# Performance work log

Measured on AMD Instinct MI355X. Metric: run time of the kernel, lower is better.

Reference implementation:

```python
import jax, jax.numpy as jnp
import numpy as np

B, F, D, OUT = 1024, 256, 256, 128
EXP = [10, 25]          # expansion_rates
CUM = [1, 10]           # cum_expansion_rates


def setup_inputs() -> dict:
    key = jax.random.key(0)
    ks = jax.random.split(key, 12)
    s = 0.05
    return {
        "h0": jax.random.normal(ks[0], (B, 1, F), jnp.float32),
        "h1": jax.random.normal(ks[1], (B, EXP[0], F), jnp.float32),
        "h2": jax.random.normal(ks[2], (B, EXP[0] * EXP[1], F), jnp.float32),
        "mask0": (jax.random.uniform(ks[3], (B, 1, EXP[0], 1)) < 0.9).astype(jnp.float32),
        "mask1": (jax.random.uniform(ks[4], (B, EXP[0], EXP[1], 1)) < 0.9).astype(jnp.float32),
        "W_self0": jax.random.normal(ks[5], (D, F), jnp.float32) * s,
        "W_neigh0": jax.random.normal(ks[6], (D, F), jnp.float32) * s,
        "W_pool0": jax.random.normal(ks[7], (D, D), jnp.float32) * s,
        "W_self1": jax.random.normal(ks[8], (D, 2 * D), jnp.float32) * s,
        "W_neigh1": jax.random.normal(ks[9], (D, 2 * D), jnp.float32) * s,
        "W_pool1": jax.random.normal(ks[10], (D, D), jnp.float32) * s,
        "W_out": jax.random.normal(ks[11], (OUT, 2 * D), jnp.float32) * s,
    }


def _sage_layer(x_self, x_neigh, mask, Ws, Wn, Wp):
    # x_self: (B, P, Fin), x_neigh: (B, P, S, Fin), mask: (B, P, S, 1)
    h_self = x_self @ Ws.T                                  # (B, P, D)
    h_neigh = jax.nn.relu(x_neigh @ Wn.T) * mask            # (B, P, S, D)
    h_pool = jnp.max(h_neigh, axis=-2) @ Wp.T               # (B, P, D) -- max pooling
    return jnp.concatenate([h_self, h_pool], axis=-1)       # (B, P, 2D)


def reference(h0, h1, h2, mask0, mask1,
              W_self0, W_neigh0, W_pool0,
              W_self1, W_neigh1, W_pool1, W_out):
    states = [h0, h1, h2]
    masks = [mask0, mask1]
    layers = [(W_self0, W_neigh0, W_pool0), (W_self1, W_neigh1, W_pool1)]
    layer_input_sizes = [F, 2 * D]
    depth = 2
    for i, (Ws, Wn, Wp) in enumerate(layers):
        fin = layer_input_sizes[i]
        for j in range(depth - i):
            x_self = states[j]
            x_neigh = states[j + 1].reshape(-1, CUM[j], EXP[j], fin)
            m = masks[j].reshape(-1, CUM[j], EXP[j], 1)
            states[j] = _sage_layer(x_self, x_neigh, m, Ws, Wn, Wp)
    return states[0][:, 0] @ W_out.T  # (B, OUT)
```

## Files before the change

### kernel.cpp

```cpp
#include <hip/hip_runtime.h>


typedef __bf16 bf16_t;
typedef bf16_t bf16x8 __attribute__((ext_vector_type(8)));
typedef float  f32x4  __attribute__((ext_vector_type(4)));

__device__ inline bf16x8 cvt8(const float4 a, const float4 b) {
  bf16x8 t;
  t[0]=(bf16_t)a.x; t[1]=(bf16_t)a.y; t[2]=(bf16_t)a.z; t[3]=(bf16_t)a.w;
  t[4]=(bf16_t)b.x; t[5]=(bf16_t)b.y; t[6]=(bf16_t)b.z; t[7]=(bf16_t)b.w;
  return t;
}

__global__ __launch_bounds__(256) void cvt_bf16(
    const float* __restrict__ s, bf16_t* __restrict__ d, int n) {
  const int i = (blockIdx.x * 256 + threadIdx.x) * 8;
  if (i < n) {
    const float4 a = *(const float4*)(s + i);
    const float4 b = *(const float4*)(s + i + 4);
    *(bf16x8*)(d + i) = cvt8(a, b);
  }
}

__device__ inline void gload_lds16(const bf16_t* g, bf16x8* l) {
  __builtin_amdgcn_global_load_lds(
      (const __attribute__((address_space(1))) unsigned int*)g,
      (__attribute__((address_space(3))) unsigned int*)l, 16, 0, 0);
}

template<typename AT> struct PreA {
  float4 lo, hi;
  __device__ void fetch(const AT* p) { lo = *(const float4*)p; hi = *(const float4*)(p + 4); }
  __device__ bf16x8 get() const { return cvt8(lo, hi); }
};
template<> struct PreA<bf16_t> {
  bf16x8 v;
  __device__ void fetch(const bf16_t* p) { v = *(const bf16x8*)p; }
  __device__ bf16x8 get() const { return v; }
};

template<int S, int PR, int P, int K, typename AT>
__global__ __launch_bounds__(256) void pool_mfma(
    const AT* __restrict__ A, const bf16_t* __restrict__ W,
    const float* __restrict__ mask, bf16_t* __restrict__ out)
{
  constexpr int ROWS = P * PR;
  constexpr int PM   = ROWS / 16;
  constexpr int MTP  = PR / 16;
  constexpr int T    = K / 32;
  __shared__ bf16x8 Blds[2][1024];
  __shared__ bf16x8 Alds[2][ROWS * 4];
  __shared__ float  mlds[ROWS];

  const int tid  = threadIdx.x;
  const int lane = tid & 63, wv = tid >> 6, quad = lane >> 4, lrow = lane & 15;
  const long p0  = (long)blockIdx.x * P;

  if (tid < P * S) mlds[(tid / S) * PR + (tid % S)] = mask[p0 * S + tid];

  const bf16_t* wptr[4];
#pragma unroll
  for (int j = 0; j < 4; ++j) {
    const int n = ((tid >> 6) + j * 4) * 16 + (tid & 15);
    wptr[j] = W + (long)n * K + ((tid >> 4) & 3) * 8;
  }
  const int wbase = (tid >> 6) * 64;

  const int mr = (tid >> 6) * 16 + (tid & 15);
  const int pp = mr / PR, rr = mr % PR;
  const long grow = (p0 + pp) * (long)S + (rr < S ? rr : S - 1);
  const AT* aptr = A + grow * (long)K + ((tid >> 4) & 3) * 8;

  f32x4 acc[PM][4];
#pragma unroll
  for (int pm = 0; pm < PM; ++pm)
#pragma unroll
    for (int nl = 0; nl < 4; ++nl) acc[pm][nl] = (f32x4){0.f, 0.f, 0.f, 0.f};

  PreA<AT> a0, apre[2];
  a0.fetch(aptr);
#pragma unroll
  for (int j = 0; j < 4; ++j) gload_lds16(wptr[j], &Blds[0][wbase + j * 256]);
  apre[0].fetch(aptr + 32);
  apre[1].fetch(aptr + 64);
  Alds[0][tid] = a0.get();
  __syncthreads();

#pragma unroll
  for (int i = 0; i < T; ++i) {
    const int cur = i & 1, nxt = cur ^ 1;
    if (i + 1 < T) {
#pragma unroll
      for (int j = 0; j < 4; ++j)
        gload_lds16(wptr[j] + (i + 1) * 32, &Blds[nxt][wbase + j * 256]);
    }
    bf16x8 bfr[4];
#pragma unroll
    for (int nl = 0; nl < 4; ++nl)
      bfr[nl] = Blds[cur][((wv * 4 + nl) * 4 + quad) * 16 + lrow];
#pragma unroll
    for (int pm = 0; pm < PM; ++pm) {
      const bf16x8 afr = Alds[cur][(pm * 4 + quad) * 16 + lrow];
#pragma unroll
      for (int nl = 0; nl < 4; ++nl)
        acc[pm][nl] = __builtin_amdgcn_mfma_f32_16x16x32_bf16(
            afr, bfr[nl], acc[pm][nl], 0, 0, 0);
    }
    if (i + 1 < T) {
      Alds[nxt][tid] = apre[i & 1].get();
      if (i + 3 < T) apre[i & 1].fetch(aptr + (i + 3) * 32);
      __syncthreads();
    }
  }

#pragma unroll
  for (int p = 0; p < P; ++p) {
#pragma unroll
    for (int nl = 0; nl < 4; ++nl) {
      float m = 0.f;
#pragma unroll
      for (int mt = 0; mt < MTP; ++mt) {
        const f32x4 v = acc[p * MTP + mt][nl];
#pragma unroll
        for (int reg = 0; reg < 4; ++reg) {
          const int row = mt * 16 + quad * 4 + reg;
          if (row < S)
            m = fmaxf(m, fmaxf(v[reg], 0.f) * mlds[p * PR + row]);
        }
      }
      m = fmaxf(m, __shfl_xor(m, 16));
      m = fmaxf(m, __shfl_xor(m, 32));
      if (lane < 16)
        out[(p0 + p) * 256 + wv * 64 + nl * 16 + lrow] = (bf16_t)m;
    }
  }
}

template<int MT, int N, int K, typename OT>
__global__ __launch_bounds__(256) void plain_mfma(
    const bf16_t* __restrict__ A0, const bf16_t* __restrict__ W0, int c0,
    const bf16_t* __restrict__ A1, const bf16_t* __restrict__ W1, int c1,
    OT* __restrict__ out, int ldc)
{
  constexpr int NTW    = N / 64;
  constexpr int BSLOTS = N * 4;
  constexpr int BPT    = BSLOTS / 256;
  constexpr int ROWS   = MT * 16;
  constexpr int ASLOTS = ROWS * 4;
  constexpr int T      = K / 32;
  __shared__ bf16x8 Blds[2][BSLOTS];
  __shared__ bf16x8 Alds[2][ASLOTS];

  const bf16_t* __restrict__ A = blockIdx.y ? A1 : A0;
  const bf16_t* __restrict__ W = blockIdx.y ? W1 : W0;
  const int coff = blockIdx.y ? c1 : c0;

  const int tid  = threadIdx.x;
  const int lane = tid & 63, wv = tid >> 6, quad = lane >> 4, lrow = lane & 15;
  const long r0  = (long)blockIdx.x * ROWS;

  const bf16_t* wptr[BPT];
#pragma unroll
  for (int j = 0; j < BPT; ++j) {
    const int n = ((tid >> 6) + j * 4) * 16 + (tid & 15);
    wptr[j] = W + (long)n * K + ((tid >> 4) & 3) * 8;
  }
  const int wbase = (tid >> 6) * 64;

  const bool aact = tid < ASLOTS;
  const int  mr   = (tid >> 6) * 16 + (tid & 15);
  const bf16_t* aptr = A + (aact ? (r0 + mr) * (long)K + ((tid >> 4) & 3) * 8 : 0);

  f32x4 acc[MT][NTW];
#pragma unroll
  for (int mt = 0; mt < MT; ++mt)
#pragma unroll
    for (int nl = 0; nl < NTW; ++nl) acc[mt][nl] = (f32x4){0.f, 0.f, 0.f, 0.f};

  PreA<bf16_t> a0p, apre[2];
  if (aact) a0p.fetch(aptr);
#pragma unroll
  for (int j = 0; j < BPT; ++j) gload_lds16(wptr[j], &Blds[0][wbase + j * 256]);
  if (aact) {
    apre[0].fetch(aptr + 32);
    apre[1].fetch(aptr + 64);
    Alds[0][tid] = a0p.get();
  }
  __syncthreads();

#pragma unroll
  for (int i = 0; i < T; ++i) {
    const int cur = i & 1, nxt = cur ^ 1;
    if (i + 1 < T) {
#pragma unroll
      for (int j = 0; j < BPT; ++j)
        gload_lds16(wptr[j] + (i + 1) * 32, &Blds[nxt][wbase + j * 256]);
    }
    bf16x8 bfr[NTW];
#pragma unroll
    for (int nl = 0; nl < NTW; ++nl)
      bfr[nl] = Blds[cur][((wv * NTW + nl) * 4 + quad) * 16 + lrow];
#pragma unroll
    for (int mt = 0; mt < MT; ++mt) {
      const bf16x8 afr = Alds[cur][(mt * 4 + quad) * 16 + lrow];
#pragma unroll
      for (int nl = 0; nl < NTW; ++nl)
        acc[mt][nl] = __builtin_amdgcn_mfma_f32_16x16x32_bf16(
            afr, bfr[nl], acc[mt][nl], 0, 0, 0);
    }
    if (i + 1 < T) {
      if (aact) {
        Alds[nxt][tid] = apre[i & 1].get();
        if (i + 3 < T) apre[i & 1].fetch(aptr + (i + 3) * 32);
      }
      __syncthreads();
    }
  }

#pragma unroll
  for (int mt = 0; mt < MT; ++mt)
#pragma unroll
    for (int nl = 0; nl < NTW; ++nl) {
      const f32x4 v = acc[mt][nl];
      const int col = coff + (wv * NTW + nl) * 16 + lrow;
#pragma unroll
      for (int reg = 0; reg < 4; ++reg) {
        const long row = r0 + mt * 16 + quad * 4 + reg;
        out[row * (long)ldc + col] = (OT)v[reg];
      }
    }
}

extern "C" void kernel_launch(void* const* d_in, const int* in_sizes, int n_in,
                              void* d_out, int out_size, void* d_ws, size_t ws_size,
                              hipStream_t stream) {
  const float* h0f   = (const float*)d_in[0];
  const float* h1f   = (const float*)d_in[1];
  const float* h2    = (const float*)d_in[2];
  const float* mask0 = (const float*)d_in[3];
  const float* mask1 = (const float*)d_in[4];
  const float* Wf[7] = { (const float*)d_in[5], (const float*)d_in[6],
                         (const float*)d_in[7], (const float*)d_in[8],
                         (const float*)d_in[9], (const float*)d_in[10],
                         (const float*)d_in[11] };
  const int   Wn[7]  = { 65536, 65536, 65536, 131072, 131072, 65536, 65536 };
  float* out = (float*)d_out;

  bf16_t* p = (bf16_t*)d_ws;
  bf16_t* Wb[7];
  for (int i = 0; i < 7; ++i) { Wb[i] = p; p += Wn[i]; }
  bf16_t* h0b = p;      p += 262144;
  bf16_t* h1b = p;      p += 2621440;
  bf16_t* pooled1  = p; p += 10240L * 256;
  bf16_t* states1  = p; p += 10240L * 512;
  bf16_t* pooled0  = p; p += 1024L * 256;
  bf16_t* states0  = p; p += 1024L * 512;
  bf16_t* pooled1b = p; p += 1024L * 256;
  bf16_t* states0b = p; p += 1024L * 512;

  const bf16_t *Ws0 = Wb[0], *Wn0 = Wb[1], *Wp0 = Wb[2], *Ws1 = Wb[3],
               *Wn1 = Wb[4], *Wp1 = Wb[5], *Wout = Wb[6];
  const dim3 blk(256);

  for (int i = 0; i < 7; ++i)
    hipLaunchKernelGGL(cvt_bf16, dim3(Wn[i] / 2048), blk, 0, stream, Wf[i], Wb[i], Wn[i]);
  hipLaunchKernelGGL(cvt_bf16, dim3(128),  blk, 0, stream, h0f, h0b, 262144);
  hipLaunchKernelGGL(cvt_bf16, dim3(1280), blk, 0, stream, h1f, h1b, 2621440);

  hipLaunchKernelGGL((pool_mfma<25, 32, 2, 256, float>), dim3(5120), blk, 0, stream,
                     h2, Wn0, mask1, pooled1);
  hipLaunchKernelGGL((pool_mfma<10, 16, 4, 256, bf16_t>), dim3(256), blk, 0, stream,
                     h1b, Wn0, mask0, pooled0);
  hipLaunchKernelGGL((plain_mfma<4, 256, 256, bf16_t>), dim3(160, 2), blk, 0, stream,
                     h1b, Ws0, 0, pooled1, Wp0, 256, states1, 512);
  hipLaunchKernelGGL((plain_mfma<1, 256, 256, bf16_t>), dim3(64, 2), blk, 0, stream,
                     h0b, Ws0, 0, pooled0, Wp0, 256, states0, 512);
  hipLaunchKernelGGL((pool_mfma<10, 16, 4, 512, bf16_t>), dim3(256), blk, 0, stream,
                     states1, Wn1, mask0, pooled1b);
  hipLaunchKernelGGL((plain_mfma<1, 256, 512, bf16_t>), dim3(64, 1), blk, 0, stream,
                     states0, Ws1, 0, states0, Ws1, 0, states0b, 512);
  hipLaunchKernelGGL((plain_mfma<1, 256, 256, bf16_t>), dim3(64, 1), blk, 0, stream,
                     pooled1b, Wp1, 256, pooled1b, Wp1, 256, states0b, 512);
  hipLaunchKernelGGL((plain_mfma<1, 128, 512, float>), dim3(64, 1), blk, 0, stream,
                     states0b, Wout, 0, states0b, Wout, 0, out, 128);
}
```

Measured before the change: 539.1 us.

## Fuse both layer-0 neighbor pooling passes into one persistent kernel with LDS-resident weights

```diff
diff --git a/kernel.cpp b/kernel.cpp
--- a/kernel.cpp
+++ b/kernel.cpp
@@ -38,6 +38,133 @@
   __device__ void fetch(const bf16_t* p) { v = *(const bf16x8*)p; }
   __device__ bf16x8 get() const { return v; }
 };
+
+__global__ __launch_bounds__(512, 2) void pool_fused(
+    const float* __restrict__ A1, const bf16_t* __restrict__ A2,
+    const bf16_t* __restrict__ W,
+    const float* __restrict__ mk1, const float* __restrict__ mk0,
+    bf16_t* __restrict__ out1, bf16_t* __restrict__ out2)
+{
+  __shared__ bf16x8 Wlds[8192];
+  const int tid  = threadIdx.x;
+  const int lane = tid & 63, wv = tid >> 6, quad = lane >> 4, lrow = lane & 15;
+
+#pragma unroll
+  for (int it = 0; it < 16; ++it) {
+    const int s  = it * 512 + tid;
+    const int kt = s >> 10, nt = (s >> 6) & 15, q = (s >> 4) & 3, lr = s & 15;
+    gload_lds16(W + ((nt * 16 + lr) << 8) + kt * 32 + q * 8,
+                &Wlds[it * 512 + wv * 64]);
+  }
+  __syncthreads();
+
+  const int gw = blockIdx.x * 8 + wv;
+
+  f32x4  acc[2][16];
+  float4 blo[2][2], bhi[2][2];
+
+  long p = gw;
+  const float* a0 = A1 + (p * 25 + lrow) * 256 + quad * 8;
+  const float* a1 = A1 + (p * 25 + (lrow > 8 ? 24 : 16 + lrow)) * 256 + quad * 8;
+
+#define ISS1(sl, kt_) \
+    { blo[sl][0] = *(const float4*)(a0 + (kt_) * 32); \
+      bhi[sl][0] = *(const float4*)(a0 + (kt_) * 32 + 4); \
+      blo[sl][1] = *(const float4*)(a1 + (kt_) * 32); \
+      bhi[sl][1] = *(const float4*)(a1 + (kt_) * 32 + 4); }
+
+  ISS1(0, 0); ISS1(1, 1);
+
+#pragma unroll 1
+  for (int t = 0; t < 5; ++t) {
+    const long pc = p;
+    float mk[2][4];
+#pragma unroll
+    for (int m2 = 0; m2 < 2; ++m2)
+#pragma unroll
+      for (int r = 0; r < 4; ++r) {
+        const int row = m2 * 16 + quad * 4 + r;
+        mk[m2][r] = row < 25 ? mk1[pc * 25 + row] : 0.f;
+      }
+#pragma unroll
+    for (int nt = 0; nt < 16; ++nt) {
+      acc[0][nt] = (f32x4){0.f, 0.f, 0.f, 0.f};
+      acc[1][nt] = (f32x4){0.f, 0.f, 0.f, 0.f};
+    }
+#pragma unroll
+    for (int kt = 0; kt < 8; ++kt) {
+      const bf16x8 af0 = cvt8(blo[kt & 1][0], bhi[kt & 1][0]);
+      const bf16x8 af1 = cvt8(blo[kt & 1][1], bhi[kt & 1][1]);
+      if (kt < 6) ISS1(kt & 1, kt + 2);
+#pragma unroll
+      for (int nt = 0; nt < 16; ++nt) {
+        const bf16x8 bfr = Wlds[((kt * 16 + nt) * 4 + quad) * 16 + lrow];
+        acc[0][nt] = __builtin_amdgcn_mfma_f32_16x16x32_bf16(af0, bfr, acc[0][nt], 0, 0, 0);
+        acc[1][nt] = __builtin_amdgcn_mfma_f32_16x16x32_bf16(af1, bfr, acc[1][nt], 0, 0, 0);
+      }
+    }
+    p += 2048;
+    if (t < 4) {
+      a0 = A1 + (p * 25 + lrow) * 256 + quad * 8;
+      a1 = A1 + (p * 25 + (lrow > 8 ? 24 : 16 + lrow)) * 256 + quad * 8;
+      ISS1(0, 0); ISS1(1, 1);
+    }
+#pragma unroll
+    for (int nt = 0; nt < 16; ++nt) {
+      float m = 0.f;
+#pragma unroll
+      for (int m2 = 0; m2 < 2; ++m2) {
+        const f32x4 v = acc[m2][nt];
+#pragma unroll
+        for (int r = 0; r < 4; ++r)
+          m = fmaxf(m, fmaxf(v[r], 0.f) * mk[m2][r]);
+      }
+      m = fmaxf(m, __shfl_xor(m, 16));
+      m = fmaxf(m, __shfl_xor(m, 32));
+      if (lane < 16) out1[pc * 256 + nt * 16 + lrow] = (bf16_t)m;
+    }
+  }
+#undef ISS1
+
+  if (gw < 1024) {
+    const long p2 = gw;
+    const bf16_t* ab = A2 + (p2 * 10 + (lrow > 9 ? 9 : lrow)) * 256 + quad * 8;
+    bf16x8 bb0 = *(const bf16x8*)(ab);
+    bf16x8 bb1 = *(const bf16x8*)(ab + 32);
+    float mk2[4];
+#pragma unroll
+    for (int r = 0; r < 4; ++r) {
+      const int row = quad * 4 + r;
+      mk2[r] = row < 10 ? mk0[p2 * 10 + row] : 0.f;
+    }
+#pragma unroll
+    for (int nt = 0; nt < 16; ++nt) acc[0][nt] = (f32x4){0.f, 0.f, 0.f, 0.f};
+#pragma unroll
+    for (int kt = 0; kt < 8; ++kt) {
+      const bf16x8 af = (kt & 1) ? bb1 : bb0;
+      if (kt < 6) {
+        if (kt & 1) bb1 = *(const bf16x8*)(ab + (kt + 2) * 32);
+        else        bb0 = *(const bf16x8*)(ab + (kt + 2) * 32);
+      }
+#pragma unroll
+      for (int nt = 0; nt < 16; ++nt) {
+        const bf16x8 bfr = Wlds[((kt * 16 + nt) * 4 + quad) * 16 + lrow];
+        acc[0][nt] = __builtin_amdgcn_mfma_f32_16x16x32_bf16(af, bfr, acc[0][nt], 0, 0, 0);
+      }
+    }
+#pragma unroll
+    for (int nt = 0; nt < 16; ++nt) {
+      float m = 0.f;
+      const f32x4 v = acc[0][nt];
+#pragma unroll
+      for (int r = 0; r < 4; ++r)
+        m = fmaxf(m, fmaxf(v[r], 0.f) * mk2[r]);
+      m = fmaxf(m, __shfl_xor(m, 16));
+      m = fmaxf(m, __shfl_xor(m, 32));
+      if (lane < 16) out2[p2 * 256 + nt * 16 + lrow] = (bf16_t)m;
+    }
+  }
+}
 
 template<int S, int PR, int P, int K, typename AT>
 __global__ __launch_bounds__(256) void pool_mfma(
@@ -267,10 +394,8 @@
   hipLaunchKernelGGL(cvt_bf16, dim3(128),  blk, 0, stream, h0f, h0b, 262144);
   hipLaunchKernelGGL(cvt_bf16, dim3(1280), blk, 0, stream, h1f, h1b, 2621440);
 
-  hipLaunchKernelGGL((pool_mfma<25, 32, 2, 256, float>), dim3(5120), blk, 0, stream,
-                     h2, Wn0, mask1, pooled1);
-  hipLaunchKernelGGL((pool_mfma<10, 16, 4, 256, bf16_t>), dim3(256), blk, 0, stream,
-                     h1b, Wn0, mask0, pooled0);
+  hipLaunchKernelGGL(pool_fused, dim3(256), dim3(512), 0, stream,
+                     h2, h1b, Wn0, mask1, mask0, pooled1, pooled0);
   hipLaunchKernelGGL((plain_mfma<4, 256, 256, bf16_t>), dim3(160, 2), blk, 0, stream,
                      h1b, Ws0, 0, pooled1, Wp0, 256, states1, 512);
   hipLaunchKernelGGL((plain_mfma<1, 256, 256, bf16_t>), dim3(64, 2), blk, 0, stream,
```

New measurement: 804.6 us. +49.3%, slower.
